# Kernel tuning notes

Hardware: AMD Instinct MI355X
Metric: run time of the kernel (lower is better)

## Reference

```python
import jax, jax.numpy as jnp
import numpy as np

EPS = 1e-3       # sinkhorn eps (init kwarg)
MAX_ITER = 100   # init kwarg

B, N, H, W = 16, 1024, 32, 32

def setup_inputs() -> dict:
    key = jax.random.key(0)
    k1, k2 = jax.random.split(key)
    x = jax.random.normal(k1, (B, N, H, W), dtype=jnp.float32)
    y = jax.random.normal(k2, (B, N, H, W), dtype=jnp.float32)
    return {"x": x, "y": y}

def _l2_normalize(a, axis=-1, eps=1e-12):
    # matches F.normalize(p=2): divide by max(norm, eps)
    n = jnp.sqrt(jnp.sum(a * a, axis=axis, keepdims=True))
    return a / jnp.maximum(n, eps)

def reference(x, y):
    b, n = x.shape[0], x.shape[1]
    xf = _l2_normalize(x.reshape(b, n, -1))          # [B,N,D], unit rows
    yf = _l2_normalize(y.reshape(b, n, -1))
    # cosine similarity of unit vectors == dot product -> GEMM instead of
    # the O(N^2 D) broadcasted intermediate in the torch source (same math)
    cost = 1.0 - jnp.einsum('bnd,bmd->bnm', xf, yf)  # [B,N,N]
    cost = cost / jnp.max(cost)                      # global max, as in torch .max()

    u0 = jnp.full((b, n), 1.0 / n, dtype=cost.dtype)
    v0 = jnp.full((b, n), 1.0 / n, dtype=cost.dtype)

    def step(carry, _):
        u, v = carry
        u = 1.0 / (jnp.einsum('bnm,bm->bn', cost, v) + EPS)
        v = 1.0 / (jnp.einsum('bnm,bn->bm', cost, u) + EPS)
        return (u, v), None

    (u, v), _ = jax.lax.scan(step, (u0, v0), None, length=MAX_ITER)

    # sum over both point dims of u_i * C_ij * v_j, then mean over batch
    distance = jnp.einsum('bn,bnm,bm->b', u, cost, v)
    return jnp.mean(distance)
```

## Files before the change

### kernel.cpp

```cpp
#include <hip/hip_runtime.h>

#define NBATCH 16
#define NPTS   1024
#define NDIM   1024
#define EPSI   1e-3f
#define NWAVES 8
#define QSCALE 127.5f

typedef __attribute__((ext_vector_type(8))) short short8;
typedef __attribute__((ext_vector_type(4))) float f32x4;

__device__ __forceinline__ unsigned short f2bf(float f) {
  union { float f; unsigned u; } v; v.f = f;
  unsigned r = v.u + 0x7fffu + ((v.u >> 16) & 1u);
  return (unsigned short)(r >> 16);
}

__device__ __forceinline__ float ld_agent(const float* p) {
  return __hip_atomic_load(p, __ATOMIC_RELAXED, __HIP_MEMORY_SCOPE_AGENT);
}
__device__ __forceinline__ void st_agent(float* p, float v) {
  __hip_atomic_store(p, v, __ATOMIC_RELAXED, __HIP_MEMORY_SCOPE_AGENT);
}

__global__ __launch_bounds__(256) void norm_kernel(const float* __restrict__ x,
                                                   const float* __restrict__ y,
                                                   unsigned short* __restrict__ xf,
                                                   unsigned short* __restrict__ yf) {
  int row = blockIdx.x;
  const float* src; unsigned short* dst;
  if (row < NBATCH * NPTS) { src = x; dst = xf; }
  else { row -= NBATCH * NPTS; src = y; dst = yf; }
  src += (size_t)row * NDIM; dst += (size_t)row * NDIM;
  const int t = threadIdx.x;
  float4 val = ((const float4*)src)[t];
  float ss = val.x*val.x + val.y*val.y + val.z*val.z + val.w*val.w;
  #pragma unroll
  for (int o = 32; o; o >>= 1) ss += __shfl_xor(ss, o, 64);
  __shared__ float wsum[4];
  if ((t & 63) == 0) wsum[t >> 6] = ss;
  __syncthreads();
  float tot = wsum[0] + wsum[1] + wsum[2] + wsum[3];
  float inv = 1.0f / fmaxf(sqrtf(tot), 1e-12f);
  ushort4 o4;
  o4.x = f2bf(val.x * inv); o4.y = f2bf(val.y * inv);
  o4.z = f2bf(val.z * inv); o4.w = f2bf(val.w * inv);
  ((ushort4*)dst)[t] = o4;
}

#define GLD_LDS16(g, l) __builtin_amdgcn_global_load_lds( \
    (const __attribute__((address_space(1))) unsigned int*)(g), \
    (__attribute__((address_space(3))) unsigned int*)(l), 16, 0, 0)

__device__ __forceinline__ unsigned char q8(float cv) {
  float t = cv * QSCALE + 0.5f;
  t = fminf(fmaxf(t, 0.f), 255.f);
  return (unsigned char)(int)t;
}

__global__ __launch_bounds__(256) void gemm_cost(const unsigned short* __restrict__ A,
                                                 const unsigned short* __restrict__ B,
                                                 unsigned char* __restrict__ Cq,
                                                 unsigned char* __restrict__ CTq,
                                                 unsigned* __restrict__ cmax_bits) {
  const int b = blockIdx.z;
  const int bm = blockIdx.y * 128, bn = blockIdx.x * 128;
  const int t = threadIdx.x, lane = t & 63, wv = t >> 6;
  const int wm = (wv & 1) * 64, wn = (wv >> 1) * 64;
  __shared__ unsigned short As[128 * 32];
  __shared__ unsigned short Bs[128 * 32];
  f32x4 acc[4][4];
  #pragma unroll
  for (int i = 0; i < 4; ++i)
    #pragma unroll
    for (int j = 0; j < 4; ++j) acc[i][j] = (f32x4){0.f, 0.f, 0.f, 0.f};

  const unsigned short* gA = A + (size_t)b*NPTS*NDIM + (size_t)(bm + (t >> 2))*NDIM + (t & 3)*8;
  const unsigned short* gB = B + (size_t)b*NPTS*NDIM + (size_t)(bn + (t >> 2))*NDIM + (t & 3)*8;
  const int ar = lane & 15, ak = (lane >> 4) * 8;

  for (int k0 = 0; k0 < NDIM; k0 += 32) {
    GLD_LDS16(gA + k0,             As + t*8);
    GLD_LDS16(gA + 64*NDIM + k0,   As + 2048 + t*8);
    GLD_LDS16(gB + k0,             Bs + t*8);
    GLD_LDS16(gB + 64*NDIM + k0,   Bs + 2048 + t*8);
    __syncthreads();
    short8 af[4], bq[4];
    #pragma unroll
    for (int i = 0; i < 4; ++i) af[i] = *(const short8*)(As + (wm + i*16 + ar)*32 + ak);
    #pragma unroll
    for (int j = 0; j < 4; ++j) bq[j] = *(const short8*)(Bs + (wn + j*16 + ar)*32 + ak);
    #pragma unroll
    for (int i = 0; i < 4; ++i)
      #pragma unroll
      for (int j = 0; j < 4; ++j)
        acc[i][j] = __builtin_amdgcn_mfma_f32_16x16x32_bf16(af[i], bq[j], acc[i][j], 0, 0, 0);
    __syncthreads();
  }

  float mx = 0.f;
  const int cr = (lane >> 4) * 4, cc = lane & 15;
  unsigned char* Cb = Cq  + (size_t)b * NPTS * NPTS;
  unsigned char* Tb = CTq + (size_t)b * NPTS * NPTS;
  #pragma unroll
  for (int i = 0; i < 4; ++i) {
    #pragma unroll
    for (int j = 0; j < 4; ++j) {
      const int row0 = bm + wm + i*16 + cr;
      const int col  = bn + wn + j*16 + cc;
      #pragma unroll
      for (int r = 0; r < 4; ++r) {
        float cv = 1.0f - acc[i][j][r];
        mx = fmaxf(mx, cv);
        unsigned char qv = q8(cv);
        Cb[(size_t)(row0 + r) * NPTS + col] = qv;
        Tb[(size_t)col * NPTS + row0 + r]   = qv;
      }
    }
  }
  #pragma unroll
  for (int o = 32; o; o >>= 1) mx = fmaxf(mx, __shfl_xor(mx, o, 64));
  if (lane == 0) atomicMax(cmax_bits, __float_as_uint(mx));
}


__device__ __forceinline__ void batch_barrier(unsigned* bar, unsigned target) {
  __syncthreads();
  if (threadIdx.x == 0) {
    __hip_atomic_fetch_add(bar, 1u, __ATOMIC_RELEASE, __HIP_MEMORY_SCOPE_AGENT);
    while (__hip_atomic_load(bar, __ATOMIC_RELAXED, __HIP_MEMORY_SCOPE_AGENT) < target)
      __builtin_amdgcn_s_sleep(1);
    asm volatile("" ::: "memory");
  }
  __syncthreads();
}

__device__ __forceinline__ void prefetch32(const unsigned char* __restrict__ rowp,
                                           unsigned* r) {
  #pragma unroll
  for (int mi = 0; mi < 32; ++mi)
    r[mi] = *(const unsigned*)(rowp + (size_t)mi * NPTS);
}

__device__ __forceinline__ void stage_gbuf(const float* __restrict__ srcp,
                                           float* gbuf, int rb, int w, int lane,
                                           float invc2) {
  if (lane < 32) {
    int m = rb + w * 32 + lane;
    float s = ld_agent(&srcp[0*NPTS + m]) + ld_agent(&srcp[1*NPTS + m])
            + ld_agent(&srcp[2*NPTS + m]) + ld_agent(&srcp[3*NPTS + m]);
    gbuf[w * 32 + lane] = 1.0f / (s * invc2 + EPSI);
  }
}

__device__ __forceinline__ float4 compute32(const unsigned* r, const float* gbase) {
  float a0 = 0.f, a1 = 0.f, a2 = 0.f, a3 = 0.f;
  #pragma unroll
  for (int mi = 0; mi < 32; ++mi) {
    unsigned q = r[mi];
    float g = gbase[mi];
    a0 += (float)(q & 0xffu) * g;
    a1 += (float)((q >> 8) & 0xffu) * g;
    a2 += (float)((q >> 16) & 0xffu) * g;
    a3 += (float)(q >> 24) * g;
  }
  return make_float4(a0, a1, a2, a3);
}

__global__ __launch_bounds__(512) void sinkhorn_kernel(
    const unsigned char* __restrict__ Cq, const unsigned char* __restrict__ CTq,
    float* __restrict__ u_part, float* __restrict__ v_part,
    unsigned* __restrict__ bar, float* __restrict__ dist,
    const unsigned* __restrict__ cmax_bits)
{
  const int wg = blockIdx.x;
  const int b = wg & (NBATCH - 1);
  const int s = wg >> 4;
  const int a = s & 3, j = s >> 2;
  const int ob = a * 256, rb = j * 256;
  const int tid = threadIdx.x, lane = tid & 63, w = tid >> 6;

  __shared__ float gbuf[256];
  __shared__ float red[NWAVES][256];
  __shared__ float dred[NWAVES];

  const float cmax = __uint_as_float(*cmax_bits);
  const float invc2 = 1.0f / (QSCALE * cmax);
  const unsigned char* rowC  = Cq  + (size_t)b*NPTS*NPTS + (size_t)(rb + w*32)*NPTS + ob + lane*4;
  const unsigned char* rowCT = CTq + (size_t)b*NPTS*NPTS + (size_t)(rb + w*32)*NPTS + ob + lane*4;
  float* upb = u_part + b * 4 * NPTS;
  float* vpb = v_part + b * 4 * NPTS;
  unsigned* barb = bar + b * 64;

  unsigned rA[32], rB[32];

  prefetch32(rowCT, rA);
  if (tid < 64) {
    float iv = ((float)NPTS - EPSI) * QSCALE * cmax * 0.25f;
    #pragma unroll
    for (int k = 0; k < 4; ++k) st_agent(&vpb[k*NPTS + s*64 + tid], iv);
  }
  unsigned bt = 16;
  batch_barrier(barb, bt); bt += 16;

  for (int it = 0; it < 100; ++it) {
    stage_gbuf(vpb, gbuf, rb, w, lane, invc2);
    prefetch32(rowC, rB);
    {
      float4 acc = compute32(rA, &gbuf[w * 32]);
      ((float4*)&red[w][lane * 4])[0] = acc;
      __syncthreads();
      if (tid < 256) {
        float ssum = 0.f;
        #pragma unroll
        for (int ww = 0; ww < NWAVES; ++ww) ssum += red[ww][tid];
        st_agent(&upb[j*NPTS + ob + tid], ssum);
      }
    }
    batch_barrier(barb, bt); bt += 16;

    stage_gbuf(upb, gbuf, rb, w, lane, invc2);
    prefetch32(rowCT, rA);
    {
      float4 acc = compute32(rB, &gbuf[w * 32]);
      ((float4*)&red[w][lane * 4])[0] = acc;
      __syncthreads();
      if (tid < 256) {
        float ssum = 0.f;
        #pragma unroll
        for (int ww = 0; ww < NWAVES; ++ww) ssum += red[ww][tid];
        st_agent(&vpb[j*NPTS + ob + tid], ssum);
      }
    }
    batch_barrier(barb, bt); bt += 16;
  }

  stage_gbuf(vpb, gbuf, rb, w, lane, invc2);
  {
    float4 acc = compute32(rA, &gbuf[w * 32]);
    ((float4*)&red[w][lane * 4])[0] = acc;
    __syncthreads();
    float term = 0.f;
    if (tid < 256) {
      float ssum = 0.f;
      #pragma unroll
      for (int ww = 0; ww < NWAVES; ++ww) ssum += red[ww][tid];
      int n = ob + tid;
      float uq = ld_agent(&upb[0*NPTS + n]) + ld_agent(&upb[1*NPTS + n])
               + ld_agent(&upb[2*NPTS + n]) + ld_agent(&upb[3*NPTS + n]);
      float un = 1.0f / (uq * invc2 + EPSI);
      term = un * ssum * invc2;
    }
    #pragma unroll
    for (int o = 32; o; o >>= 1) term += __shfl_xor(term, o, 64);
    if (lane == 0) dred[w] = term;
    __syncthreads();
    if (tid == 0) {
      float d = 0.f;
      #pragma unroll
      for (int ww = 0; ww < NWAVES; ++ww) d += dred[ww];
      atomicAdd(dist + b, d);
    }
  }
}

__global__ void finalize_kernel(const float* __restrict__ dist, float* __restrict__ out) {
  if (threadIdx.x == 0) {
    float s = 0.f;
    for (int i = 0; i < NBATCH; ++i) s += dist[i];
    out[0] = s * (1.0f / NBATCH);
  }
}

extern "C" void kernel_launch(void* const* d_in, const int* in_sizes, int n_in,
                              void* d_out, int out_size, void* d_ws, size_t ws_size,
                              hipStream_t stream) {
  (void)in_sizes; (void)n_in; (void)out_size; (void)ws_size;
  const float* x = (const float*)d_in[0];
  const float* y = (const float*)d_in[1];
  float* out = (float*)d_out;
  char* ws = (char*)d_ws;

  unsigned* cmax_bits = (unsigned*)ws;
  unsigned* bar       = (unsigned*)(ws + 4096);
  float*    dist      = (float*)(ws + 8192);
  float*    u_part    = (float*)(ws + 65536);
  float*    v_part    = (float*)(ws + 65536 + 262144);
  const size_t MB = 1u << 20;
  unsigned short* xf = (unsigned short*)(ws + 1*MB);
  unsigned short* yf = (unsigned short*)(ws + 33*MB);
  unsigned char*  C  = (unsigned char*)(ws + 65*MB);
  unsigned char*  CT = (unsigned char*)(ws + 81*MB);

  hipMemsetAsync(d_ws, 0, 65536, stream);

  hipLaunchKernelGGL(norm_kernel, dim3(2 * NBATCH * NPTS), dim3(256), 0, stream, x, y, xf, yf);
  hipLaunchKernelGGL(gemm_cost, dim3(8, 8, NBATCH), dim3(256), 0, stream, xf, yf, C, CT, cmax_bits);
  hipLaunchKernelGGL(sinkhorn_kernel, dim3(256), dim3(512), 0, stream, C, CT, u_part, v_part, bar, dist, cmax_bits);
  hipLaunchKernelGGL(finalize_kernel, dim3(1), dim3(64), 0, stream, dist, out);
}
```

Baseline: 1.180 ms.

## Replace batch barriers with sign-flag polling and row-per-wave sinkhorn partition

Removes the atomic counter barrier between Sinkhorn half-steps. Each workgroup now owns 64 full rows and writes final u/v values directly, tagging each value with an alternating sign bit so consumers spin on the data itself. Each wave keeps whole rows of C and C^T in registers and reduces with wave shuffles, which drops the partial-sum buffers and the LDS cross-wave reduction. The cost is per-element spinning on 64-bit loads, and correctness relies on the sign-flag protocol and on the workspace being zeroed.

```diff
diff --git a/kernel.cpp b/kernel.cpp
--- a/kernel.cpp
+++ b/kernel.cpp
@@ -4,7 +4,6 @@
 #define NPTS   1024
 #define NDIM   1024
 #define EPSI   1e-3f
-#define NWAVES 8
 #define QSCALE 127.5f
 
 typedef __attribute__((ext_vector_type(8))) short short8;
@@ -21,6 +20,9 @@
 }
 __device__ __forceinline__ void st_agent(float* p, float v) {
   __hip_atomic_store(p, v, __ATOMIC_RELAXED, __HIP_MEMORY_SCOPE_AGENT);
+}
+__device__ __forceinline__ unsigned long long ld_agent64(const unsigned long long* p) {
+  return __hip_atomic_load(p, __ATOMIC_RELAXED, __HIP_MEMORY_SCOPE_AGENT);
 }
 
 __global__ __launch_bounds__(256) void norm_kernel(const float* __restrict__ x,
@@ -124,143 +126,143 @@
 }
 
 
-__device__ __forceinline__ void batch_barrier(unsigned* bar, unsigned target) {
-  __syncthreads();
-  if (threadIdx.x == 0) {
-    __hip_atomic_fetch_add(bar, 1u, __ATOMIC_RELEASE, __HIP_MEMORY_SCOPE_AGENT);
-    while (__hip_atomic_load(bar, __ATOMIC_RELAXED, __HIP_MEMORY_SCOPE_AGENT) < target)
-      __builtin_amdgcn_s_sleep(1);
-    asm volatile("" ::: "memory");
-  }
-  __syncthreads();
-}
-
-__device__ __forceinline__ void prefetch32(const unsigned char* __restrict__ rowp,
-                                           unsigned* r) {
-  #pragma unroll
-  for (int mi = 0; mi < 32; ++mi)
-    r[mi] = *(const unsigned*)(rowp + (size_t)mi * NPTS);
-}
-
-__device__ __forceinline__ void stage_gbuf(const float* __restrict__ srcp,
-                                           float* gbuf, int rb, int w, int lane,
-                                           float invc2) {
-  if (lane < 32) {
-    int m = rb + w * 32 + lane;
-    float s = ld_agent(&srcp[0*NPTS + m]) + ld_agent(&srcp[1*NPTS + m])
-            + ld_agent(&srcp[2*NPTS + m]) + ld_agent(&srcp[3*NPTS + m]);
-    gbuf[w * 32 + lane] = 1.0f / (s * invc2 + EPSI);
-  }
-}
-
-__device__ __forceinline__ float4 compute32(const unsigned* r, const float* gbase) {
-  float a0 = 0.f, a1 = 0.f, a2 = 0.f, a3 = 0.f;
-  #pragma unroll
-  for (int mi = 0; mi < 32; ++mi) {
-    unsigned q = r[mi];
-    float g = gbase[mi];
-    a0 += (float)(q & 0xffu) * g;
-    a1 += (float)((q >> 8) & 0xffu) * g;
-    a2 += (float)((q >> 16) & 0xffu) * g;
-    a3 += (float)(q >> 24) * g;
-  }
-  return make_float4(a0, a1, a2, a3);
-}
+__device__ __forceinline__ float dot16(uint4 q, f32x4 g0, f32x4 g1, f32x4 g2, f32x4 g3) {
+  float a = 0.f;
+  a += (float)( q.x        & 0xffu) * g0.x;
+  a += (float)((q.x >>  8) & 0xffu) * g0.y;
+  a += (float)((q.x >> 16) & 0xffu) * g0.z;
+  a += (float)( q.x >> 24         ) * g0.w;
+  a += (float)( q.y        & 0xffu) * g1.x;
+  a += (float)((q.y >>  8) & 0xffu) * g1.y;
+  a += (float)((q.y >> 16) & 0xffu) * g1.z;
+  a += (float)( q.y >> 24         ) * g1.w;
+  a += (float)( q.z        & 0xffu) * g2.x;
+  a += (float)((q.z >>  8) & 0xffu) * g2.y;
+  a += (float)((q.z >> 16) & 0xffu) * g2.z;
+  a += (float)( q.z >> 24         ) * g2.w;
+  a += (float)( q.w        & 0xffu) * g3.x;
+  a += (float)((q.w >>  8) & 0xffu) * g3.y;
+  a += (float)((q.w >> 16) & 0xffu) * g3.z;
+  a += (float)( q.w >> 24         ) * g3.w;
+  return a;
+}
+
+__device__ __forceinline__ void poll_stage(const float* __restrict__ src, float* dst,
+                                           int tid, int i0, bool expneg) {
+  const unsigned long long* p0 = (const unsigned long long*)(src + 2 * tid);
+  const unsigned long long SGN = 0x8000000080000000ull;
+  unsigned long long t = ld_agent64(p0);
+  int spins = 0;
+  if (expneg) {
+    while ((t & SGN) != SGN) {
+      if (++spins > 32) __builtin_amdgcn_s_sleep(1);
+      t = ld_agent64(p0);
+    }
+  } else {
+    while ((t & SGN) != 0ull ||
+           (t & 0x7fffffffull) == 0ull ||
+           (t & 0x7fffffff00000000ull) == 0ull) {
+      if (++spins > 32) __builtin_amdgcn_s_sleep(1);
+      t = ld_agent64(p0);
+    }
+  }
+  union { unsigned u; float f; } lo, hi;
+  lo.u = (unsigned)t & 0x7fffffffu;
+  hi.u = (unsigned)(t >> 32) & 0x7fffffffu;
+  dst[i0]     = lo.f;
+  dst[i0 + 1] = hi.f;
+}
+
+#define LOAD_G(buf)                                          \
+  const f32x4 g0 = *(const f32x4*)&buf[      lane * 4];      \
+  const f32x4 g1 = *(const f32x4*)&buf[256 + lane * 4];      \
+  const f32x4 g2 = *(const f32x4*)&buf[512 + lane * 4];      \
+  const f32x4 g3 = *(const f32x4*)&buf[768 + lane * 4];
 
 __global__ __launch_bounds__(512) void sinkhorn_kernel(
     const unsigned char* __restrict__ Cq, const unsigned char* __restrict__ CTq,
-    float* __restrict__ u_part, float* __restrict__ v_part,
-    unsigned* __restrict__ bar, float* __restrict__ dist,
-    const unsigned* __restrict__ cmax_bits)
+    float* __restrict__ ubuf, float* __restrict__ vbuf,
+    float* __restrict__ dist, const unsigned* __restrict__ cmax_bits)
 {
   const int wg = blockIdx.x;
   const int b = wg & (NBATCH - 1);
   const int s = wg >> 4;
-  const int a = s & 3, j = s >> 2;
-  const int ob = a * 256, rb = j * 256;
+  const int ob = s * 64;
   const int tid = threadIdx.x, lane = tid & 63, w = tid >> 6;
 
-  __shared__ float gbuf[256];
-  __shared__ float red[NWAVES][256];
-  __shared__ float dred[NWAVES];
-
-  const float cmax = __uint_as_float(*cmax_bits);
+  __shared__ __align__(16) float gb0[1024];
+  __shared__ __align__(16) float gb1[1024];
+
+  const float cmax  = __uint_as_float(*cmax_bits);
   const float invc2 = 1.0f / (QSCALE * cmax);
-  const unsigned char* rowC  = Cq  + (size_t)b*NPTS*NPTS + (size_t)(rb + w*32)*NPTS + ob + lane*4;
-  const unsigned char* rowCT = CTq + (size_t)b*NPTS*NPTS + (size_t)(rb + w*32)*NPTS + ob + lane*4;
-  float* upb = u_part + b * 4 * NPTS;
-  float* vpb = v_part + b * 4 * NPTS;
-  unsigned* barb = bar + b * 64;
-
-  unsigned rA[32], rB[32];
-
-  prefetch32(rowCT, rA);
-  if (tid < 64) {
-    float iv = ((float)NPTS - EPSI) * QSCALE * cmax * 0.25f;
-    #pragma unroll
-    for (int k = 0; k < 4; ++k) st_agent(&vpb[k*NPTS + s*64 + tid], iv);
-  }
-  unsigned bt = 16;
-  batch_barrier(barb, bt); bt += 16;
-
+
+  uint4 mc[8], mt[8];
+  {
+    const unsigned char* cb = Cq  + (size_t)b * NPTS * NPTS;
+    const unsigned char* tb = CTq + (size_t)b * NPTS * NPTS;
+    #pragma unroll
+    for (int p = 0; p < 8; ++p) {
+      const size_t off = (size_t)(ob + p * 8 + w) * NPTS + lane * 16;
+      mc[p] = *(const uint4*)(cb + off);
+      mt[p] = *(const uint4*)(tb + off);
+    }
+  }
+
+  float* ub = ubuf + b * NPTS;
+  float* vb = vbuf + b * NPTS;
+
+  if (tid < 64) st_agent(&vb[ob + tid], 1.0f / (float)NPTS);
+
+  const int i0 = ((tid >> 1) & 3) * 256 + (tid >> 3) * 4 + (tid & 1) * 2;
+  float uk[8];
+
+  #pragma unroll 1
   for (int it = 0; it < 100; ++it) {
-    stage_gbuf(vpb, gbuf, rb, w, lane, invc2);
-    prefetch32(rowC, rB);
+    const float sgn = (it & 1) ? 1.f : -1.f;
+
+    poll_stage(vb, gb0, tid, i0, (it & 1) != 0);
+    __syncthreads();
     {
-      float4 acc = compute32(rA, &gbuf[w * 32]);
-      ((float4*)&red[w][lane * 4])[0] = acc;
-      __syncthreads();
-      if (tid < 256) {
-        float ssum = 0.f;
+      LOAD_G(gb0);
+      #pragma unroll
+      for (int p = 0; p < 8; ++p) {
+        float acc = dot16(mc[p], g0, g1, g2, g3);
         #pragma unroll
-        for (int ww = 0; ww < NWAVES; ++ww) ssum += red[ww][tid];
-        st_agent(&upb[j*NPTS + ob + tid], ssum);
+        for (int o = 32; o; o >>= 1) acc += __shfl_xor(acc, o, 64);
+        const float val = 1.0f / (acc * invc2 + EPSI);
+        uk[p] = val;
+        if (lane == 0) st_agent(&ub[ob + p * 8 + w], val * sgn);
       }
     }
-    batch_barrier(barb, bt); bt += 16;
-
-    stage_gbuf(upb, gbuf, rb, w, lane, invc2);
-    prefetch32(rowCT, rA);
+
+    poll_stage(ub, gb1, tid, i0, (it & 1) == 0);
+    __syncthreads();
     {
-      float4 acc = compute32(rB, &gbuf[w * 32]);
-      ((float4*)&red[w][lane * 4])[0] = acc;
-      __syncthreads();
-      if (tid < 256) {
-        float ssum = 0.f;
+      LOAD_G(gb1);
+      #pragma unroll
+      for (int p = 0; p < 8; ++p) {
+        float acc = dot16(mt[p], g0, g1, g2, g3);
         #pragma unroll
-        for (int ww = 0; ww < NWAVES; ++ww) ssum += red[ww][tid];
-        st_agent(&vpb[j*NPTS + ob + tid], ssum);
+        for (int o = 32; o; o >>= 1) acc += __shfl_xor(acc, o, 64);
+        const float val = 1.0f / (acc * invc2 + EPSI);
+        if (lane == 0) st_agent(&vb[ob + p * 8 + w], val * sgn);
       }
     }
-    batch_barrier(barb, bt); bt += 16;
-  }
-
-  stage_gbuf(vpb, gbuf, rb, w, lane, invc2);
+  }
+
+  poll_stage(vb, gb0, tid, i0, false);
+  __syncthreads();
   {
-    float4 acc = compute32(rA, &gbuf[w * 32]);
-    ((float4*)&red[w][lane * 4])[0] = acc;
-    __syncthreads();
+    LOAD_G(gb0);
     float term = 0.f;
-    if (tid < 256) {
-      float ssum = 0.f;
-      #pragma unroll
-      for (int ww = 0; ww < NWAVES; ++ww) ssum += red[ww][tid];
-      int n = ob + tid;
-      float uq = ld_agent(&upb[0*NPTS + n]) + ld_agent(&upb[1*NPTS + n])
-               + ld_agent(&upb[2*NPTS + n]) + ld_agent(&upb[3*NPTS + n]);
-      float un = 1.0f / (uq * invc2 + EPSI);
-      term = un * ssum * invc2;
-    }
-    #pragma unroll
-    for (int o = 32; o; o >>= 1) term += __shfl_xor(term, o, 64);
-    if (lane == 0) dred[w] = term;
-    __syncthreads();
-    if (tid == 0) {
-      float d = 0.f;
-      #pragma unroll
-      for (int ww = 0; ww < NWAVES; ++ww) d += dred[ww];
-      atomicAdd(dist + b, d);
-    }
+    #pragma unroll
+    for (int p = 0; p < 8; ++p) {
+      float acc = dot16(mc[p], g0, g1, g2, g3);
+      #pragma unroll
+      for (int o = 32; o; o >>= 1) acc += __shfl_xor(acc, o, 64);
+      term += uk[p] * acc;
+    }
+    if (lane == 0) atomicAdd(dist + b, term * invc2);
   }
 }
 
@@ -282,20 +284,19 @@
   char* ws = (char*)d_ws;
 
   unsigned* cmax_bits = (unsigned*)ws;
-  unsigned* bar       = (unsigned*)(ws + 4096);
   float*    dist      = (float*)(ws + 8192);
-  float*    u_part    = (float*)(ws + 65536);
-  float*    v_part    = (float*)(ws + 65536 + 262144);
+  float*    vbuf      = (float*)(ws + 65536);
+  float*    ubuf      = (float*)(ws + 131072);
   const size_t MB = 1u << 20;
   unsigned short* xf = (unsigned short*)(ws + 1*MB);
   unsigned short* yf = (unsigned short*)(ws + 33*MB);
   unsigned char*  C  = (unsigned char*)(ws + 65*MB);
   unsigned char*  CT = (unsigned char*)(ws + 81*MB);
 
-  hipMemsetAsync(d_ws, 0, 65536, stream);
+  hipMemsetAsync(d_ws, 0, 262144, stream);
 
   hipLaunchKernelGGL(norm_kernel, dim3(2 * NBATCH * NPTS), dim3(256), 0, stream, x, y, xf, yf);
   hipLaunchKernelGGL(gemm_cost, dim3(8, 8, NBATCH), dim3(256), 0, stream, xf, yf, C, CT, cmax_bits);
-  hipLaunchKernelGGL(sinkhorn_kernel, dim3(256), dim3(512), 0, stream, C, CT, u_part, v_part, bar, dist, cmax_bits);
+  hipLaunchKernelGGL(sinkhorn_kernel, dim3(256), dim3(512), 0, stream, C, CT, ubuf, vbuf, dist, cmax_bits);
   hipLaunchKernelGGL(finalize_kernel, dim3(1), dim3(64), 0, stream, dist, out);
 }
```

Result: slower. 1.756 ms (+48.8%).
